# Kernel optimization log

Hardware: AMD Instinct MI355X
Metric: run time of the kernel (lower is better)

## Reference

```python
import jax, jax.numpy as jnp
import numpy as np

N, IN_DIM, OUT_DIM = 16384, 256, 128

def setup_inputs() -> dict:
    key = jax.random.key(0)
    ks = jax.random.split(key, 7)
    s_in = 1.0 / np.sqrt(IN_DIM)
    return {
        "x": jax.random.normal(ks[0], (N, IN_DIM), dtype=jnp.float32),
        "Wq": jax.random.uniform(ks[1], (IN_DIM, OUT_DIM), jnp.float32, -s_in, s_in),
        "bq": jax.random.uniform(ks[2], (OUT_DIM,), jnp.float32, -s_in, s_in),
        "Wk": jax.random.uniform(ks[3], (IN_DIM, OUT_DIM), jnp.float32, -s_in, s_in),
        "bk": jax.random.uniform(ks[4], (OUT_DIM,), jnp.float32, -s_in, s_in),
        "Wv": jax.random.uniform(ks[5], (IN_DIM, OUT_DIM), jnp.float32, -s_in, s_in),
        "bv": jax.random.uniform(ks[6], (OUT_DIM,), jnp.float32, -s_in, s_in),
    }

def reference(x, Wq, bq, Wk, bk, Wv, bv):
    # QKV projections: [N, out_dim]
    q = x @ Wq + bq
    k = x @ Wk + bk
    v = x @ Wv + bv
    # Unscaled dot-product affinity [N, N], row softmax, weighted sum of V.
    affinity = jax.nn.softmax(q @ k.T, axis=-1)
    return affinity @ v
```

## Files before the change

### kernel.cpp

```cpp
#include <hip/hip_runtime.h>

typedef _Float16 f16;
typedef _Float16 f16x8 __attribute__((ext_vector_type(8)));
typedef float f32x4 __attribute__((ext_vector_type(4)));
typedef float f32x16 __attribute__((ext_vector_type(16)));

#define MFMA16(a, b, c) __builtin_amdgcn_mfma_f32_16x16x32_f16((a), (b), (c), 0, 0, 0)
#define MFMA32(a, b, c) __builtin_amdgcn_mfma_f32_32x32x16_f16((a), (b), (c), 0, 0, 0)
#define LOG2E 1.44269504088896340736f
#define SHIFT_L2 28.8539008178f

#define NROWS 16384
#define INDIM 256
#define ODIM 128
#define NQT 128

__global__ __launch_bounds__(256) void prep_kernel(
    const float* __restrict__ Wq, const float* __restrict__ Wk, const float* __restrict__ Wv,
    f16* __restrict__ WqT, f16* __restrict__ WkT, f16* __restrict__ WvT) {
    int w = blockIdx.x >> 5;
    int local = blockIdx.x & 31;
    const float* W = (w == 0) ? Wq : ((w == 1) ? Wk : Wv);
    f16* WT = (w == 0) ? WqT : ((w == 1) ? WkT : WvT);
    int j0 = local * 1024 + threadIdx.x;
#pragma unroll
    for (int t = 0; t < 4; t++) {
        int j = j0 + t * 256;
        int n = j >> 8;
        int k = j & 255;
        WT[j] = (f16)W[k * ODIM + n];
    }
}

__global__ __launch_bounds__(256) void proj_kernel(
    const float* __restrict__ x,
    const f16* __restrict__ WqT, const f16* __restrict__ WkT, const f16* __restrict__ WvT,
    const float* __restrict__ bq, const float* __restrict__ bk, const float* __restrict__ bv,
    f16* __restrict__ Qh, f16* __restrict__ Kh, f16* __restrict__ Vt) {
    int blk = blockIdx.x;
    int wave = threadIdx.x >> 6;
    int lane = threadIdx.x & 63;
    int l16 = lane & 15, quad = lane >> 4;

    if (blk < 256) {
        int r0 = blk * 64 + wave * 16;
        f16x8 ax[8];
        const float* xp = x + (size_t)(r0 + l16) * INDIM + quad * 8;
#pragma unroll
        for (int kc = 0; kc < 8; kc++) {
            f32x4 u = *(const f32x4*)(xp + kc * 32);
            f32x4 v = *(const f32x4*)(xp + kc * 32 + 4);
            f16x8 t;
            t[0] = (f16)u[0]; t[1] = (f16)u[1]; t[2] = (f16)u[2]; t[3] = (f16)u[3];
            t[4] = (f16)v[0]; t[5] = (f16)v[1]; t[6] = (f16)v[2]; t[7] = (f16)v[3];
            ax[kc] = t;
        }
#pragma unroll
        for (int nt = 0; nt < 8; nt++) {
            f32x4 aq = {0.f, 0.f, 0.f, 0.f}, ak = {0.f, 0.f, 0.f, 0.f};
            const f16* wq = WqT + (nt * 16 + l16) * INDIM + quad * 8;
            const f16* wk = WkT + (nt * 16 + l16) * INDIM + quad * 8;
#pragma unroll
            for (int kc = 0; kc < 8; kc++) {
                f16x8 bqf = *(const f16x8*)(wq + kc * 32);
                f16x8 bkf = *(const f16x8*)(wk + kc * 32);
                aq = MFMA16(ax[kc], bqf, aq);
                ak = MFMA16(ax[kc], bkf, ak);
            }
            int col = nt * 16 + l16;
            float biasq = bq[col], biask = bk[col];
#pragma unroll
            for (int r = 0; r < 4; r++) {
                int row = r0 + quad * 4 + r;
                Qh[(size_t)row * ODIM + col] = (f16)(aq[r] + biasq);
                Kh[(size_t)row * ODIM + col] = (f16)(ak[r] + biask);
            }
        }
    } else {
        int i0 = (blk - 256) * 64 + wave * 16;
        f16x8 bx[8];
        const float* xp = x + (size_t)(i0 + l16) * INDIM + quad * 8;
#pragma unroll
        for (int kc = 0; kc < 8; kc++) {
            f32x4 u = *(const f32x4*)(xp + kc * 32);
            f32x4 v = *(const f32x4*)(xp + kc * 32 + 4);
            f16x8 t;
            t[0] = (f16)u[0]; t[1] = (f16)u[1]; t[2] = (f16)u[2]; t[3] = (f16)u[3];
            t[4] = (f16)v[0]; t[5] = (f16)v[1]; t[6] = (f16)v[2]; t[7] = (f16)v[3];
            bx[kc] = t;
        }
#pragma unroll
        for (int dt = 0; dt < 8; dt++) {
            f32x4 acc = {0.f, 0.f, 0.f, 0.f};
            const f16* wv = WvT + (dt * 16 + l16) * INDIM + quad * 8;
#pragma unroll
            for (int kc = 0; kc < 8; kc++) {
                f16x8 a = *(const f16x8*)(wv + kc * 32);
                acc = MFMA16(a, bx[kc], acc);
            }
#pragma unroll
            for (int r = 0; r < 4; r++) {
                int d = dt * 16 + quad * 4 + r;
                Vt[(size_t)d * NROWS + i0 + l16] = (f16)(acc[r] + bv[d]);
            }
        }
    }
}

__global__ __launch_bounds__(256, 2) void flash_kernel(
    const f16* __restrict__ Qh, const f16* __restrict__ Kh, const f16* __restrict__ Vt,
    float* __restrict__ Opart, float* __restrict__ lbuf, float* __restrict__ Out,
    int nsplit, int niter) {
    int blk = blockIdx.x;
    int qt = blk & (NQT - 1);
    int sp = blk >> 7;
    int tid = threadIdx.x;
    int wave = tid >> 6;
    int lane = tid & 63;
    int l32 = lane & 31;
    int h = lane >> 5;

    __shared__ __align__(16) f16 Kl[2][64 * 136];
    __shared__ __align__(16) f16 Vl[2][128 * 72];

    int rowbase = qt * 128 + wave * 32;

    f16x8 qf[8];
    {
        const f16* qp = Qh + (size_t)(rowbase + l32) * ODIM + h * 8;
#pragma unroll
        for (int ks = 0; ks < 8; ks++) qf[ks] = *(const f16x8*)(qp + ks * 16);
    }

    f32x16 o[4];
#pragma unroll
    for (int dt = 0; dt < 4; dt++)
#pragma unroll
        for (int g = 0; g < 16; g++) o[dt][g] = 0.f;
    float l_r = 0.f;

    int kr_row = tid >> 2, kr_c = (tid & 3) * 32;
    int vr_d = tid >> 1, vr_h = (tid & 1) * 32;
    const f16* kgp = Kh + (size_t)kr_row * ODIM + kr_c;
    const f16* vgp = Vt + (size_t)vr_d * NROWS + vr_h;

    int j0 = sp * (niter * 64);

    f16x8 kr[4], vr[4];
    {
        const f16* kp = kgp + (size_t)j0 * ODIM;
        const f16* vp = vgp + j0;
#pragma unroll
        for (int i = 0; i < 4; i++) {
            kr[i] = *(const f16x8*)(kp + i * 8);
            vr[i] = *(const f16x8*)(vp + i * 8);
        }
        f16* kd = Kl[0] + kr_row * 136 + kr_c;
        f16* vd = Vl[0] + vr_d * 72 + vr_h;
#pragma unroll
        for (int i = 0; i < 4; i++) {
            *(f16x8*)(kd + i * 8) = kr[i];
            *(f16x8*)(vd + i * 8) = vr[i];
        }
        if (1 < niter) {
            const f16* kp1 = kgp + (size_t)(j0 + 64) * ODIM;
            const f16* vp1 = vgp + (j0 + 64);
#pragma unroll
            for (int i = 0; i < 4; i++) {
                kr[i] = *(const f16x8*)(kp1 + i * 8);
                vr[i] = *(const f16x8*)(vp1 + i * 8);
            }
        }
    }
    __syncthreads();

    for (int it = 0; it < niter; ++it) {
        int p = it & 1;
        int pk[2][8];
#pragma unroll
        for (int ct = 0; ct < 2; ct++) {
            f32x16 st;
#pragma unroll
            for (int g = 0; g < 16; g++) st[g] = 0.f;
            const f16* kp = Kl[p] + (ct * 32 + l32) * 136 + h * 8;
#pragma unroll
            for (int ks = 0; ks < 8; ks++) {
                f16x8 kf = *(const f16x8*)(kp + ks * 16);
                st = MFMA32(kf, qf[ks], st);
            }
#pragma unroll
            for (int w = 0; w < 8; w++) {
                float a = __builtin_amdgcn_exp2f(fmaf(st[2 * w], LOG2E, -SHIFT_L2));
                float b = __builtin_amdgcn_exp2f(fmaf(st[2 * w + 1], LOG2E, -SHIFT_L2));
                l_r += a + b;
                pk[ct][w] = __builtin_bit_cast(int, __builtin_amdgcn_cvt_pkrtz(a, b));
            }
        }
        f16x8 pf[4];
#pragma unroll
        for (int ks = 0; ks < 4; ks++) {
            int ct = ks >> 1, b = (ks & 1) * 4;
            int off0 = h ? pk[ct][b] : pk[ct][b + 2];
            int off1 = h ? pk[ct][b + 1] : pk[ct][b + 3];
            int R0 = __shfl_xor(off0, 32, 64);
            int R1 = __shfl_xor(off1, 32, 64);
            union { int i[4]; f16x8 v; } u;
            u.i[0] = h ? R0 : pk[ct][b];
            u.i[1] = h ? R1 : pk[ct][b + 1];
            u.i[2] = h ? pk[ct][b + 2] : R0;
            u.i[3] = h ? pk[ct][b + 3] : R1;
            pf[ks] = u.v;
        }
#pragma unroll
        for (int dt = 0; dt < 4; dt++) {
            const f16* vp = Vl[p] + (dt * 32 + l32) * 72 + h * 8;
#pragma unroll
            for (int ks = 0; ks < 4; ks++) {
                f16x8 vf = *(const f16x8*)(vp + ks * 16);
                o[dt] = MFMA32(vf, pf[ks], o[dt]);
            }
        }
        if (it + 1 < niter) {
            f16* kd = Kl[1 - p] + kr_row * 136 + kr_c;
            f16* vd = Vl[1 - p] + vr_d * 72 + vr_h;
#pragma unroll
            for (int i = 0; i < 4; i++) {
                *(f16x8*)(kd + i * 8) = kr[i];
                *(f16x8*)(vd + i * 8) = vr[i];
            }
            if (it + 2 < niter) {
                int jn = j0 + 128;
                const f16* kp = kgp + (size_t)jn * ODIM;
                const f16* vp = vgp + jn;
#pragma unroll
                for (int i = 0; i < 4; i++) {
                    kr[i] = *(const f16x8*)(kp + i * 8);
                    vr[i] = *(const f16x8*)(vp + i * 8);
                }
            }
        }
        __syncthreads();
        j0 += 64;
    }

    l_r += __shfl_xor(l_r, 32, 64);

    if (nsplit == 1) {
        float inv = 1.f / l_r;
        float* op = Out + (size_t)(rowbase + l32) * ODIM;
#pragma unroll
        for (int dt = 0; dt < 4; dt++)
#pragma unroll
            for (int gg = 0; gg < 4; gg++) {
                f32x4 v = {o[dt][4 * gg] * inv, o[dt][4 * gg + 1] * inv,
                           o[dt][4 * gg + 2] * inv, o[dt][4 * gg + 3] * inv};
                *(f32x4*)(op + dt * 32 + 8 * gg + 4 * h) = v;
            }
    } else {
        float* op = Opart + ((size_t)sp * NROWS + rowbase + l32) * ODIM;
#pragma unroll
        for (int dt = 0; dt < 4; dt++)
#pragma unroll
            for (int gg = 0; gg < 4; gg++) {
                f32x4 v = {o[dt][4 * gg], o[dt][4 * gg + 1],
                           o[dt][4 * gg + 2], o[dt][4 * gg + 3]};
                *(f32x4*)(op + dt * 32 + 8 * gg + 4 * h) = v;
            }
        if (lane < 32)
            lbuf[(size_t)sp * NROWS + rowbase + l32] = l_r;
    }
}

__global__ __launch_bounds__(256) void merge_kernel(const float* __restrict__ Opart,
                                                    const float* __restrict__ lbuf,
                                                    float* __restrict__ out, int nsplit) {
    int idx = (blockIdx.x * 256 + threadIdx.x) * 4;
    int row = idx >> 7;
    f32x4 acc = {0.f, 0.f, 0.f, 0.f};
    float den = 0.f;
    for (int s = 0; s < nsplit; s++) {
        f32x4 v = *(const f32x4*)(Opart + (size_t)s * (NROWS * ODIM) + idx);
        acc[0] += v[0]; acc[1] += v[1]; acc[2] += v[2]; acc[3] += v[3];
        den += lbuf[(size_t)s * NROWS + row];
    }
    float inv = 1.f / den;
    f32x4 r = {acc[0] * inv, acc[1] * inv, acc[2] * inv, acc[3] * inv};
    *(f32x4*)(out + idx) = r;
}

extern "C" void kernel_launch(void* const* d_in, const int* in_sizes, int n_in,
                              void* d_out, int out_size, void* d_ws, size_t ws_size,
                              hipStream_t stream) {
    const float* x  = (const float*)d_in[0];
    const float* Wq = (const float*)d_in[1];
    const float* bq = (const float*)d_in[2];
    const float* Wk = (const float*)d_in[3];
    const float* bk = (const float*)d_in[4];
    const float* Wv = (const float*)d_in[5];
    const float* bv = (const float*)d_in[6];
    float* out = (float*)d_out;
    char* ws = (char*)d_ws;

    const size_t WT_BYTES = (size_t)ODIM * INDIM * sizeof(f16);
    const size_t QKV_BYTES = (size_t)NROWS * ODIM * sizeof(f16);
    f16* WqT = (f16*)(ws);
    f16* WkT = (f16*)(ws + WT_BYTES);
    f16* WvT = (f16*)(ws + 2 * WT_BYTES);
    f16* Qh  = (f16*)(ws + 3 * WT_BYTES);
    f16* Kh  = (f16*)(ws + 3 * WT_BYTES + QKV_BYTES);
    f16* Vt  = (f16*)(ws + 3 * WT_BYTES + 2 * QKV_BYTES);
    size_t base = 3 * WT_BYTES + 3 * QKV_BYTES;

    const size_t OPART_BYTES = (size_t)NROWS * ODIM * sizeof(float);
    const size_t L_BYTES = (size_t)NROWS * sizeof(float);

    int nsplit = 1;
    if (ws_size >= base + 4 * (OPART_BYTES + L_BYTES)) nsplit = 4;
    else if (ws_size >= base + 2 * (OPART_BYTES + L_BYTES)) nsplit = 2;

    float* Opart = (float*)(ws + base);
    float* lbuf  = (float*)(ws + base + (size_t)nsplit * OPART_BYTES);

    prep_kernel<<<96, 256, 0, stream>>>(Wq, Wk, Wv, WqT, WkT, WvT);
    proj_kernel<<<512, 256, 0, stream>>>(x, WqT, WkT, WvT, bq, bk, bv, Qh, Kh, Vt);
    flash_kernel<<<NQT * nsplit, 256, 0, stream>>>(Qh, Kh, Vt, Opart, lbuf, out, nsplit,
                                                   (NROWS / 64) / nsplit);
    if (nsplit > 1)
        merge_kernel<<<(NROWS * ODIM) / 1024, 256, 0, stream>>>(Opart, lbuf, out, nsplit);
}
```

Before: 254.5 us.

## Load K/V tiles directly to LDS with global_load_lds and XOR-swizzled layout

Replaces the register-staged double-buffered K/V prefetch with direct global-to-LDS loads issued at the start of each iteration into the other buffer. The padded LDS layout is swapped for an unpadded one with an XOR swizzle, and the fragment reads are remapped to match. The aim is to free the VGPRs held by the staged tiles, drop the explicit LDS stores, and avoid bank conflicts without padding. It depends on the swizzle and wave-uniform LDS base addressing being correct, and the async loads now rely on the existing barrier for completion.

```diff
diff --git a/kernel.cpp b/kernel.cpp
--- a/kernel.cpp
+++ b/kernel.cpp
@@ -9,6 +9,11 @@
 #define MFMA32(a, b, c) __builtin_amdgcn_mfma_f32_32x32x16_f16((a), (b), (c), 0, 0, 0)
 #define LOG2E 1.44269504088896340736f
 #define SHIFT_L2 28.8539008178f
+
+#define GLOAD_LDS16(g, l)                                              \
+    __builtin_amdgcn_global_load_lds(                                  \
+        (const __attribute__((address_space(1))) void*)(g),            \
+        (__attribute__((address_space(3))) void*)(l), 16, 0, 0)
 
 #define NROWS 16384
 #define INDIM 256
@@ -120,8 +125,8 @@
     int l32 = lane & 31;
     int h = lane >> 5;
 
-    __shared__ __align__(16) f16 Kl[2][64 * 136];
-    __shared__ __align__(16) f16 Vl[2][128 * 72];
+    __shared__ __align__(16) f16 Kl[2][64 * 128];
+    __shared__ __align__(16) f16 Vl[2][128 * 64];
 
     int rowbase = qt * 128 + wave * 32;
 
@@ -139,53 +144,51 @@
         for (int g = 0; g < 16; g++) o[dt][g] = 0.f;
     float l_r = 0.f;
 
-    int kr_row = tid >> 2, kr_c = (tid & 3) * 32;
-    int vr_d = tid >> 1, vr_h = (tid & 1) * 32;
-    const f16* kgp = Kh + (size_t)kr_row * ODIM + kr_c;
-    const f16* vgp = Vt + (size_t)vr_d * NROWS + vr_h;
+    int rK[4], cK[4], dV[4], cV[4];
+#pragma unroll
+    for (int t = 0; t < 4; t++) {
+        int s = wave * 256 + t * 64 + lane;
+        rK[t] = s >> 4;
+        cK[t] = ((s & 15) ^ (rK[t] & 7)) * 8;
+        dV[t] = s >> 3;
+        cV[t] = ((s & 7) ^ (dV[t] & 7)) * 8;
+    }
+    int rr = (l32 >> 1) & 3;
+    int hh = h ^ (l32 & 1);
 
     int j0 = sp * (niter * 64);
 
-    f16x8 kr[4], vr[4];
-    {
-        const f16* kp = kgp + (size_t)j0 * ODIM;
-        const f16* vp = vgp + j0;
-#pragma unroll
-        for (int i = 0; i < 4; i++) {
-            kr[i] = *(const f16x8*)(kp + i * 8);
-            vr[i] = *(const f16x8*)(vp + i * 8);
-        }
-        f16* kd = Kl[0] + kr_row * 136 + kr_c;
-        f16* vd = Vl[0] + vr_d * 72 + vr_h;
-#pragma unroll
-        for (int i = 0; i < 4; i++) {
-            *(f16x8*)(kd + i * 8) = kr[i];
-            *(f16x8*)(vd + i * 8) = vr[i];
-        }
-        if (1 < niter) {
-            const f16* kp1 = kgp + (size_t)(j0 + 64) * ODIM;
-            const f16* vp1 = vgp + (j0 + 64);
-#pragma unroll
-            for (int i = 0; i < 4; i++) {
-                kr[i] = *(const f16x8*)(kp1 + i * 8);
-                vr[i] = *(const f16x8*)(vp1 + i * 8);
-            }
-        }
+#pragma unroll
+    for (int t = 0; t < 4; t++) {
+        GLOAD_LDS16(Kh + (size_t)(j0 + rK[t]) * ODIM + cK[t],
+                    &Kl[0][(wave * 4 + t) * 512]);
+        GLOAD_LDS16(Vt + (size_t)dV[t] * NROWS + j0 + cV[t],
+                    &Vl[0][(wave * 4 + t) * 512]);
     }
     __syncthreads();
 
     for (int it = 0; it < niter; ++it) {
         int p = it & 1;
+        if (it + 1 < niter) {
+            int jn = j0 + 64;
+#pragma unroll
+            for (int t = 0; t < 4; t++) {
+                GLOAD_LDS16(Kh + (size_t)(jn + rK[t]) * ODIM + cK[t],
+                            &Kl[1 - p][(wave * 4 + t) * 512]);
+                GLOAD_LDS16(Vt + (size_t)dV[t] * NROWS + jn + cV[t],
+                            &Vl[1 - p][(wave * 4 + t) * 512]);
+            }
+        }
         int pk[2][8];
 #pragma unroll
         for (int ct = 0; ct < 2; ct++) {
             f32x16 st;
 #pragma unroll
             for (int g = 0; g < 16; g++) st[g] = 0.f;
-            const f16* kp = Kl[p] + (ct * 32 + l32) * 136 + h * 8;
+            const f16* kb = &Kl[p][(ct * 32 + l32) * 128 + hh * 8];
 #pragma unroll
             for (int ks = 0; ks < 8; ks++) {
-                f16x8 kf = *(const f16x8*)(kp + ks * 16);
+                f16x8 kf = *(const f16x8*)(kb + ((ks ^ rr) << 4));
                 st = MFMA32(kf, qf[ks], st);
             }
 #pragma unroll
@@ -213,30 +216,11 @@
         }
 #pragma unroll
         for (int dt = 0; dt < 4; dt++) {
-            const f16* vp = Vl[p] + (dt * 32 + l32) * 72 + h * 8;
+            const f16* vb = &Vl[p][(dt * 32 + l32) * 64 + hh * 8];
 #pragma unroll
             for (int ks = 0; ks < 4; ks++) {
-                f16x8 vf = *(const f16x8*)(vp + ks * 16);
+                f16x8 vf = *(const f16x8*)(vb + ((ks ^ rr) << 4));
                 o[dt] = MFMA32(vf, pf[ks], o[dt]);
-            }
-        }
-        if (it + 1 < niter) {
-            f16* kd = Kl[1 - p] + kr_row * 136 + kr_c;
-            f16* vd = Vl[1 - p] + vr_d * 72 + vr_h;
-#pragma unroll
-            for (int i = 0; i < 4; i++) {
-                *(f16x8*)(kd + i * 8) = kr[i];
-                *(f16x8*)(vd + i * 8) = vr[i];
-            }
-            if (it + 2 < niter) {
-                int jn = j0 + 128;
-                const f16* kp = kgp + (size_t)jn * ODIM;
-                const f16* vp = vgp + jn;
-#pragma unroll
-                for (int i = 0; i < 4; i++) {
-                    kr[i] = *(const f16x8*)(kp + i * 8);
-                    vr[i] = *(const f16x8*)(vp + i * 8);
-                }
             }
         }
         __syncthreads();
```

New measurement: 254.2 us. About the same (-0.1%).
